# Kernel tuning notes

Hardware: AMD Instinct MI355X
Metric: run time of the kernel (lower is better)

Reference implementation:

```python
import jax, jax.numpy as jnp
import numpy as np

B, C, E, K = 16, 256, 9216, 4096  # meshes, channels, max input edges, target edges (out_channel)


def setup_inputs() -> dict:
    key = jax.random.key(0)
    k1, k2 = jax.random.split(key)
    x = jax.random.normal(k1, (B, C, E), dtype=jnp.float32)
    # ragged per-mesh edge counts, all >= K so pooling target is reachable
    edges_count = E - jax.random.randint(k2, (B,), 0, 512)
    return {"x": x, "edges_count": edges_count.astype(jnp.int64), "out_channel": K}


def reference(x, edges_count, out_channel):
    # Per-mesh edge saliency: squared sum over channels (torch.sum(x**2, dim=0)).
    score = jnp.sum(x * x, axis=1)  # [B, E]
    # Mask padded (invalid) edges beyond each mesh's edges_count so they are never kept.
    valid = jnp.arange(score.shape[-1]) < edges_count[:, None]
    score = jnp.where(valid, score, -jnp.inf)
    # Greedy collapse removes the lowest-score edges until out_channel edges remain:
    # keep the out_channel highest-score edges (descending sort + mask in the original).
    _, keep_idx = jax.lax.top_k(score, out_channel)  # [B, K]
    # Preserve original edge ordering of the surviving edges (mask-based rebuild).
    keep_idx = jnp.sort(keep_idx, axis=-1)
    # Gather surviving edge features -> [B, C, K]; matches view(B, -1, out_target).
    out = jnp.take_along_axis(x, keep_idx[:, None, :], axis=2)
    return out
```

## Files before the change

### kernel.cpp

```cpp
#include <hip/hip_runtime.h>
#include <hip/hip_bf16.h>

#define B_DIM 16
#define C_DIM 256
#define E_DIM 9216
#define K_DIM 4096

__global__ __launch_bounds__(256) void score_kernel(
    const float* __restrict__ x, const void* __restrict__ ecp,
    unsigned* __restrict__ keys) {
  int tid = blockIdx.x * blockDim.x + threadIdx.x;
  int b = tid / E_DIM;
  int e = tid - b * E_DIM;

  const int* p32 = (const int*)ecp;
  long long cnt = (p32[1] == 0) ? ((const long long*)ecp)[b] : (long long)p32[b];

  const float* col = x + (size_t)b * C_DIM * E_DIM + e;
  double a0 = 0.0, a1 = 0.0, a2 = 0.0, a3 = 0.0;
#pragma unroll 8
  for (int c = 0; c < C_DIM; c += 4) {
    float v0 = col[(size_t)(c + 0) * E_DIM];
    float v1 = col[(size_t)(c + 1) * E_DIM];
    float v2 = col[(size_t)(c + 2) * E_DIM];
    float v3 = col[(size_t)(c + 3) * E_DIM];
    a0 += (double)v0 * v0;
    a1 += (double)v1 * v1;
    a2 += (double)v2 * v2;
    a3 += (double)v3 * v3;
  }
  float s = (float)((a0 + a1) + (a2 + a3));
  unsigned key = (e < cnt) ? (__float_as_uint(s) | 0x80000000u) : 0u;
  keys[tid] = key;
}

__device__ __forceinline__ void block_scan(int flag, int tid, int* wsum,
                                           int nwaves, int* excl, int* total) {
  int lane = tid & 63;
  int wid = tid >> 6;
  int v = flag;
#pragma unroll
  for (int i = 1; i < 64; i <<= 1) {
    int t = __shfl_up(v, i, 64);
    if (lane >= i) v += t;
  }
  if (lane == 63) wsum[wid] = v;
  __syncthreads();
  int base = 0, tot = 0;
  for (int w = 0; w < nwaves; w++) {
    int s = wsum[w];
    if (w < wid) base += s;
    tot += s;
  }
  *excl = base + v - flag;
  *total = tot;
  __syncthreads();
}

__global__ __launch_bounds__(512) void select_kernel(
    const unsigned* __restrict__ keys, int* __restrict__ keep) {
  __shared__ unsigned lkeys[E_DIM];
  __shared__ int hist[256];
  __shared__ int wsum[8];
  __shared__ unsigned sh_prefix;
  __shared__ int sh_remK;

  const int b = blockIdx.x;
  const int tid = threadIdx.x;
  const int bs = blockDim.x;

  for (int e = tid; e < E_DIM; e += bs) lkeys[e] = keys[b * E_DIM + e];
  __syncthreads();

  unsigned prefix = 0;
  int remK = K_DIM;
  for (int pass = 3; pass >= 0; pass--) {
    int shift = pass * 8;
    for (int i = tid; i < 256; i += bs) hist[i] = 0;
    __syncthreads();
    for (int e = tid; e < E_DIM; e += bs) {
      unsigned key = lkeys[e];
      bool cand = (pass == 3) || ((key >> (shift + 8)) == prefix);
      if (cand) atomicAdd(&hist[(key >> shift) & 255], 1);
    }
    __syncthreads();
    if (tid == 0) {
      int cum = 0;
      int bin = 255;
      for (; bin > 0; bin--) {
        if (cum + hist[bin] >= remK) break;
        cum += hist[bin];
      }
      sh_prefix = (prefix << 8) | (unsigned)bin;
      sh_remK = remK - cum;
    }
    __syncthreads();
    prefix = sh_prefix;
    remK = sh_remK;
  }

  const unsigned T = prefix;
  const int need_eq = remK;

  int eq_base = 0, keep_base = 0;
  const int nwaves = bs >> 6;
  for (int base_e = 0; base_e < E_DIM; base_e += bs) {
    int e = base_e + tid;
    unsigned key = lkeys[e];
    int eq = (key == T) ? 1 : 0;
    int gt = (key > T) ? 1 : 0;
    int eq_excl, eq_tot;
    block_scan(eq, tid, wsum, nwaves, &eq_excl, &eq_tot);
    int kp = gt | (eq && (eq_base + eq_excl) < need_eq ? 1 : 0);
    int k_excl, k_tot;
    block_scan(kp, tid, wsum, nwaves, &k_excl, &k_tot);
    int pos = keep_base + k_excl;
    if (kp && pos < K_DIM) keep[b * K_DIM + pos] = e;
    eq_base += eq_tot;
    keep_base += k_tot;
  }
}

__global__ __launch_bounds__(256) void gather_kernel(
    const float* __restrict__ x, const int* __restrict__ keep,
    float* __restrict__ out) {
  int tid = blockIdx.x * blockDim.x + threadIdx.x;
  const int KQ = K_DIM / 4;
  int q = tid & (KQ - 1);
  int bc = tid >> 10;
  int b = bc >> 8;

  int4 idx4 = ((const int4*)(keep + b * K_DIM))[q];
  const float* row = x + (size_t)bc * E_DIM;
  float4 o;
  o.x = row[idx4.x];
  o.y = row[idx4.y];
  o.z = row[idx4.z];
  o.w = row[idx4.w];
  ((float4*)out)[tid] = o;
}

extern "C" void kernel_launch(void* const* d_in, const int* in_sizes, int n_in,
                              void* d_out, int out_size, void* d_ws,
                              size_t ws_size, hipStream_t stream) {
  const float* x = (const float*)d_in[0];
  const void* ec = d_in[1];
  float* out = (float*)d_out;

  unsigned* keys = (unsigned*)d_ws;
  int* keep = (int*)(keys + (size_t)B_DIM * E_DIM);

  score_kernel<<<(B_DIM * E_DIM) / 256, 256, 0, stream>>>(x, ec, keys);
  select_kernel<<<B_DIM, 512, 0, stream>>>(keys, keep);
  gather_kernel<<<(B_DIM * C_DIM * (K_DIM / 4)) / 256, 256, 0, stream>>>(
      x, keep, out);
}
```

Measured before the change: 323.1 us.

## Register-block select kernel with ballot-aggregated histograms and single-scan compaction

The score kernel now handles two adjacent edges per thread using float2 loads and uint2 key stores, which halves the thread count. The select kernel keeps 18 contiguous keys per thread in registers. It builds each radix histogram with wave-level ballot matching, so one leader per distinct byte does a single atomicAdd, which is meant to cut atomic contention on hot bins. The threshold bin is found with a parallel block scan instead of a serial loop in thread 0. Compaction is one packed gt/eq block scan followed by per-thread sequential writes, replacing 18 rounds of paired block scans; the cost is higher register pressure and fewer score threads for hiding latency.

```diff
diff --git a/kernel.cpp b/kernel.cpp
--- a/kernel.cpp
+++ b/kernel.cpp
@@ -5,40 +5,44 @@
 #define C_DIM 256
 #define E_DIM 9216
 #define K_DIM 4096
+#define SEL_T 512
+#define EPT   (E_DIM / SEL_T)
 
 __global__ __launch_bounds__(256) void score_kernel(
     const float* __restrict__ x, const void* __restrict__ ecp,
     unsigned* __restrict__ keys) {
   int tid = blockIdx.x * blockDim.x + threadIdx.x;
-  int b = tid / E_DIM;
-  int e = tid - b * E_DIM;
+  const int EH = E_DIM / 2;
+  int b = tid / EH;
+  int e = (tid - b * EH) * 2;
 
   const int* p32 = (const int*)ecp;
   long long cnt = (p32[1] == 0) ? ((const long long*)ecp)[b] : (long long)p32[b];
 
   const float* col = x + (size_t)b * C_DIM * E_DIM + e;
-  double a0 = 0.0, a1 = 0.0, a2 = 0.0, a3 = 0.0;
+  double a00 = 0.0, a01 = 0.0, a10 = 0.0, a11 = 0.0;
 #pragma unroll 8
-  for (int c = 0; c < C_DIM; c += 4) {
-    float v0 = col[(size_t)(c + 0) * E_DIM];
-    float v1 = col[(size_t)(c + 1) * E_DIM];
-    float v2 = col[(size_t)(c + 2) * E_DIM];
-    float v3 = col[(size_t)(c + 3) * E_DIM];
-    a0 += (double)v0 * v0;
-    a1 += (double)v1 * v1;
-    a2 += (double)v2 * v2;
-    a3 += (double)v3 * v3;
+  for (int c = 0; c < C_DIM; c += 2) {
+    float2 v0 = *(const float2*)(col + (size_t)c * E_DIM);
+    float2 v1 = *(const float2*)(col + (size_t)(c + 1) * E_DIM);
+    a00 += (double)v0.x * v0.x;
+    a10 += (double)v0.y * v0.y;
+    a01 += (double)v1.x * v1.x;
+    a11 += (double)v1.y * v1.y;
   }
-  float s = (float)((a0 + a1) + (a2 + a3));
-  unsigned key = (e < cnt) ? (__float_as_uint(s) | 0x80000000u) : 0u;
-  keys[tid] = key;
+  float s0 = (float)(a00 + a01);
+  float s1 = (float)(a10 + a11);
+  uint2 k;
+  k.x = (e + 0 < cnt) ? (__float_as_uint(s0) | 0x80000000u) : 0u;
+  k.y = (e + 1 < cnt) ? (__float_as_uint(s1) | 0x80000000u) : 0u;
+  *(uint2*)(keys + (size_t)b * E_DIM + e) = k;
 }
 
-__device__ __forceinline__ void block_scan(int flag, int tid, int* wsum,
-                                           int nwaves, int* excl, int* total) {
+__device__ __forceinline__ void block_scan(int val, int tid, int* wsum,
+                                           int* excl, int* total) {
   int lane = tid & 63;
   int wid = tid >> 6;
-  int v = flag;
+  int v = val;
 #pragma unroll
   for (int i = 1; i < 64; i <<= 1) {
     int t = __shfl_up(v, i, 64);
@@ -47,52 +51,77 @@
   if (lane == 63) wsum[wid] = v;
   __syncthreads();
   int base = 0, tot = 0;
-  for (int w = 0; w < nwaves; w++) {
+#pragma unroll
+  for (int w = 0; w < SEL_T / 64; w++) {
     int s = wsum[w];
     if (w < wid) base += s;
     tot += s;
   }
-  *excl = base + v - flag;
+  *excl = base + v - val;
   *total = tot;
   __syncthreads();
 }
 
-__global__ __launch_bounds__(512) void select_kernel(
+__global__ __launch_bounds__(SEL_T) void select_kernel(
     const unsigned* __restrict__ keys, int* __restrict__ keep) {
   __shared__ unsigned lkeys[E_DIM];
   __shared__ int hist[256];
-  __shared__ int wsum[8];
+  __shared__ int wsum[SEL_T / 64];
   __shared__ unsigned sh_prefix;
   __shared__ int sh_remK;
 
   const int b = blockIdx.x;
   const int tid = threadIdx.x;
-  const int bs = blockDim.x;
+  const int lane = tid & 63;
 
-  for (int e = tid; e < E_DIM; e += bs) lkeys[e] = keys[b * E_DIM + e];
+  {
+    const uint2* gk = (const uint2*)(keys + (size_t)b * E_DIM);
+    uint2* lk2 = (uint2*)lkeys;
+    for (int i = tid; i < E_DIM / 2; i += SEL_T) lk2[i] = gk[i];
+  }
   __syncthreads();
+
+  unsigned kreg[EPT];
+  const int base_e = tid * EPT;
+#pragma unroll
+  for (int j = 0; j < EPT; j++) kreg[j] = lkeys[base_e + j];
 
   unsigned prefix = 0;
   int remK = K_DIM;
+#pragma unroll
   for (int pass = 3; pass >= 0; pass--) {
-    int shift = pass * 8;
-    for (int i = tid; i < 256; i += bs) hist[i] = 0;
+    const int shift = pass * 8;
+    if (tid < 256) hist[tid] = 0;
     __syncthreads();
-    for (int e = tid; e < E_DIM; e += bs) {
-      unsigned key = lkeys[e];
+
+#pragma unroll
+    for (int j = 0; j < EPT; j++) {
+      unsigned key = kreg[j];
       bool cand = (pass == 3) || ((key >> (shift + 8)) == prefix);
-      if (cand) atomicAdd(&hist[(key >> shift) & 255], 1);
+      unsigned byte = (key >> shift) & 255u;
+      unsigned long long m = __ballot(cand);
+#pragma unroll
+      for (int bit = 0; bit < 8; bit++) {
+        unsigned long long bb = __ballot((byte >> bit) & 1u);
+        m &= ((byte >> bit) & 1u) ? bb : ~bb;
+      }
+      if (cand) {
+        int leader = __ffsll((unsigned long long)m) - 1;
+        if (lane == leader) atomicAdd(&hist[byte], (int)__popcll(m));
+      }
     }
     __syncthreads();
-    if (tid == 0) {
-      int cum = 0;
-      int bin = 255;
-      for (; bin > 0; bin--) {
-        if (cum + hist[bin] >= remK) break;
-        cum += hist[bin];
+
+    int h = 0;
+    if (tid < 256) h = hist[255 - tid];
+    int excl, tot;
+    block_scan(h, tid, wsum, &excl, &tot);
+    if (tid < 256) {
+      int s_incl = excl + h;
+      if (s_incl >= remK && (s_incl - h) < remK) {
+        sh_prefix = (prefix << 8) | (unsigned)(255 - tid);
+        sh_remK = remK - (s_incl - h);
       }
-      sh_prefix = (prefix << 8) | (unsigned)bin;
-      sh_remK = remK - cum;
     }
     __syncthreads();
     prefix = sh_prefix;
@@ -102,22 +131,29 @@
   const unsigned T = prefix;
   const int need_eq = remK;
 
-  int eq_base = 0, keep_base = 0;
-  const int nwaves = bs >> 6;
-  for (int base_e = 0; base_e < E_DIM; base_e += bs) {
-    int e = base_e + tid;
-    unsigned key = lkeys[e];
-    int eq = (key == T) ? 1 : 0;
-    int gt = (key > T) ? 1 : 0;
-    int eq_excl, eq_tot;
-    block_scan(eq, tid, wsum, nwaves, &eq_excl, &eq_tot);
-    int kp = gt | (eq && (eq_base + eq_excl) < need_eq ? 1 : 0);
-    int k_excl, k_tot;
-    block_scan(kp, tid, wsum, nwaves, &k_excl, &k_tot);
-    int pos = keep_base + k_excl;
-    if (kp && pos < K_DIM) keep[b * K_DIM + pos] = e;
-    eq_base += eq_tot;
-    keep_base += k_tot;
+  int gt_cnt = 0, eq_cnt = 0;
+#pragma unroll
+  for (int j = 0; j < EPT; j++) {
+    gt_cnt += (kreg[j] > T);
+    eq_cnt += (kreg[j] == T);
+  }
+  int excl, tot;
+  block_scan((gt_cnt << 16) | eq_cnt, tid, wsum, &excl, &tot);
+  int gt_b = excl >> 16;
+  int eq_b = excl & 0xFFFF;
+
+  int* kout = keep + b * K_DIM;
+#pragma unroll
+  for (int j = 0; j < EPT; j++) {
+    unsigned key = kreg[j];
+    if (key > T) {
+      int pos = gt_b + (eq_b < need_eq ? eq_b : need_eq);
+      kout[pos] = base_e + j;
+      gt_b++;
+    } else if (key == T) {
+      if (eq_b < need_eq) kout[gt_b + eq_b] = base_e + j;
+      eq_b++;
+    }
   }
 }
 
@@ -150,8 +186,8 @@
   unsigned* keys = (unsigned*)d_ws;
   int* keep = (int*)(keys + (size_t)B_DIM * E_DIM);
 
-  score_kernel<<<(B_DIM * E_DIM) / 256, 256, 0, stream>>>(x, ec, keys);
-  select_kernel<<<B_DIM, 512, 0, stream>>>(keys, keep);
+  score_kernel<<<(B_DIM * E_DIM / 2) / 256, 256, 0, stream>>>(x, ec, keys);
+  select_kernel<<<B_DIM, SEL_T, 0, stream>>>(keys, keep);
   gather_kernel<<<(B_DIM * C_DIM * (K_DIM / 4)) / 256, 256, 0, stream>>>(
       x, keep, out);
 }
```

Result: faster. 285.3 us (-11.7%).
